# Kernel tuning notes

Hardware: AMD Instinct MI355X
Metric: run time of the kernel (lower is better)

Reference implementation:

```python
import jax, jax.numpy as jnp
import numpy as np

B, C, H, W = 8, 256, 64, 64
S = H * W  # dim_spatial = 4096
DQK = 256
DV = 256


def setup_inputs() -> dict:
    key = jax.random.key(0)
    k1, k2, k3, k4, k5 = jax.random.split(key, 5)
    queries = jax.random.normal(k1, (B, DQK, H, W), dtype=jnp.float32)
    keys = jax.random.normal(k2, (B, DQK, H, W), dtype=jnp.float32)
    values = jax.random.normal(k3, (B, DV, H, W), dtype=jnp.float32)
    q_pos = jax.random.normal(k4, (1, S, DQK), dtype=jnp.float32) * 0.05  # 'random_normal' init
    k_pos = jax.random.normal(k5, (1, S, DQK), dtype=jnp.float32) * 0.05
    return {"queries": queries, "keys": keys, "values": values, "q_pos": q_pos, "k_pos": k_pos}


def reference(queries, keys, values, q_pos, k_pos):
    scale = DQK ** (-0.5)
    # NCHW -> (B, S, C)
    q = jnp.transpose(queries, (0, 2, 3, 1)).reshape(-1, S, DQK) + q_pos
    k = jnp.transpose(keys, (0, 2, 3, 1)).reshape(-1, S, DQK) + k_pos
    v = jnp.transpose(values, (0, 2, 3, 1)).reshape(-1, S, DV)
    dots = jnp.einsum('bqd,bkd->bqk', q, k) * scale  # (B, S, S)
    attn = jax.nn.softmax(dots, axis=-1)
    out = jnp.einsum('bqk,bkd->bqd', attn, v)  # (B, S, DV)
    out = jnp.transpose(out, (0, 2, 1)).reshape(values.shape)  # (B, DV, H, W)
    return out
```

## Files before the change

### kernel.cpp

```cpp
#include <hip/hip_runtime.h>
#include <hip/hip_bf16.h>

#define B_N   8
#define S_N   4096
#define D_N   256
#define QBLK  64
#define KVBLK 64
#define SCALE 0.0625f

typedef __attribute__((ext_vector_type(8)))  short bf16x8;
typedef __attribute__((ext_vector_type(16))) float f32x16;

__device__ __forceinline__ void async16(const char* g, char* l) {
  __builtin_amdgcn_global_load_lds(
      (const __attribute__((address_space(1))) void*)g,
      (__attribute__((address_space(3))) void*)l, 16, 0, 0);
}

__device__ __forceinline__ unsigned cvt_pk_bf16(float lo, float hi) {
  unsigned r;
  asm("v_cvt_pk_bf16_f32 %0, %1, %2" : "=v"(r) : "v"(lo), "v"(hi));
  return r;
}
__device__ __forceinline__ void swap32(unsigned& a, unsigned& b) {
  asm("v_permlane32_swap_b32 %0, %1" : "+v"(a), "+v"(b));
}
__device__ __forceinline__ float xhalf_max(float x) {
  float a = x, b = x;
  asm("" : "+v"(b));
  asm("v_permlane32_swap_b32 %0, %1" : "+v"(a), "+v"(b));
  return fmaxf(a, b);
}
__device__ __forceinline__ float xhalf_add(float x) {
  float a = x, b = x;
  asm("" : "+v"(b));
  asm("v_permlane32_swap_b32 %0, %1" : "+v"(a), "+v"(b));
  return a + b;
}

__global__ void prep_qk(const float* __restrict__ src, const float* __restrict__ pos,
                        __hip_bfloat16* __restrict__ dst, float mul) {
  __shared__ float tile[64][65];
  const int b  = blockIdx.z;
  const int s0 = blockIdx.x * 64;
  const int c0 = blockIdx.y * 64;
  const int t  = threadIdx.x;
  const int x  = t & 63;
  const int y4 = t >> 6;
  const float* sp = src + ((size_t)b * D_N + c0) * S_N + s0;
#pragma unroll
  for (int i = 0; i < 16; ++i) {
    int c = y4 + i * 4;
    tile[c][x] = sp[(size_t)c * S_N + x];
  }
  __syncthreads();
  __hip_bfloat16* dp = dst + ((size_t)b * S_N + s0) * D_N + c0;
  const float* pp = pos + (size_t)s0 * D_N + c0;
#pragma unroll
  for (int i = 0; i < 16; ++i) {
    int s = y4 + i * 4;
    float v = (tile[x][s] + pp[(size_t)s * D_N + x]) * mul;
    dp[(size_t)s * D_N + x] = __float2bfloat16(v);
  }
}

struct alignas(8) bf4 { __hip_bfloat16 a, b, c, d; };
__global__ void prep_v(const float* __restrict__ src, __hip_bfloat16* __restrict__ dst) {
  size_t i = (size_t)blockIdx.x * blockDim.x + threadIdx.x;
  float4 v = reinterpret_cast<const float4*>(src)[i];
  bf4 o { __float2bfloat16(v.x), __float2bfloat16(v.y),
          __float2bfloat16(v.z), __float2bfloat16(v.w) };
  *reinterpret_cast<bf4*>(dst + i * 4) = o;
}

#define LDS_BYTES 65536

__global__ __launch_bounds__(128, 1) void attn_kernel(
    const __hip_bfloat16* __restrict__ Qb, const __hip_bfloat16* __restrict__ Kb,
    const __hip_bfloat16* __restrict__ Vtb, float* __restrict__ out) {
  __shared__ __align__(16) char lds[LDS_BYTES];

  const int tid  = threadIdx.x;
  const int wave = tid >> 6;
  const int lane = tid & 63;
  const int l31  = lane & 31;
  const int h    = lane >> 5;
  const int l7   = lane & 7;

  const int lin   = blockIdx.x;
  const int b     = lin & 7;
  const int qtile = lin >> 3;
  const int q0    = qtile * QBLK + wave * 32;

  bf16x8 qf[16];
  {
    const __hip_bfloat16* qp = Qb + ((size_t)b * S_N + q0 + l31) * D_N + h * 8;
#pragma unroll
    for (int kc = 0; kc < 16; ++kc)
      qf[kc] = *reinterpret_cast<const bf16x8*>(qp + kc * 16);
  }

  f32x16 o[8];
#pragma unroll
  for (int df = 0; df < 8; ++df)
#pragma unroll
    for (int r = 0; r < 16; ++r) o[df][r] = 0.f;
  float m_ = -1e30f, l_ = 0.f;

  char* Klds = lds;
  char* Vlds = lds + 32768;
  const char* kgbase = reinterpret_cast<const char*>(Kb  + (size_t)b * S_N * D_N);
  const char* vgbase = reinterpret_cast<const char*>(Vtb + (size_t)b * D_N * S_N);

  for (int t = 0; t < S_N / KVBLK; ++t) {
    __syncthreads();
    {
      const char* kt = kgbase + (size_t)t * KVBLK * (D_N * 2);
#pragma unroll
      for (int i = 0; i < 16; ++i) {
        int c    = wave * 16 + i;
        int T    = c * 1024 + lane * 16;
        int row  = T >> 9;
        int colb = T & 511;
        async16(kt + row * 512 + (colb ^ ((row & 7) << 4)), Klds + c * 1024);
      }
      const char* vt = vgbase + (size_t)t * KVBLK * 2;
#pragma unroll
      for (int i = 0; i < 16; ++i) {
        int c    = wave * 16 + i;
        int T    = c * 1024 + lane * 16;
        int d    = T >> 7;
        int colb = T & 127;
        async16(vt + (size_t)d * (S_N * 2) + (colb ^ ((d & 7) << 4)), Vlds + c * 1024);
      }
    }
    __syncthreads();

    f32x16 se[2];
#pragma unroll
    for (int e = 0; e < 2; ++e) {
#pragma unroll
      for (int r = 0; r < 16; ++r) se[e][r] = 0.f;
      const char* kr = Klds + (e * 32 + l31) * 512;
      const int swz = l7 << 4;
#pragma unroll
      for (int kc = 0; kc < 16; ++kc) {
        bf16x8 kf = *reinterpret_cast<const bf16x8*>(kr + ((kc * 32 + h * 16) ^ swz));
        se[e] = __builtin_amdgcn_mfma_f32_32x32x16_bf16(kf, qf[kc], se[e], 0, 0, 0);
      }
    }

    float t8[8];
#pragma unroll
    for (int i = 0; i < 8; ++i)
      t8[i] = fmaxf(fmaxf(se[0][i], se[0][i + 8]), fmaxf(se[1][i], se[1][i + 8]));
    float pm = fmaxf(fmaxf(fmaxf(t8[0], t8[1]), fmaxf(t8[2], t8[3])),
                     fmaxf(fmaxf(t8[4], t8[5]), fmaxf(t8[6], t8[7])));
    float pmax = xhalf_max(pm);

    if (!__all(pmax <= m_ + 8.f)) {
      float mn = fmaxf(m_, pmax);
      float al = __expf(m_ - mn);
      m_ = mn;
      l_ *= al;
#pragma unroll
      for (int df = 0; df < 8; ++df)
#pragma unroll
        for (int r = 0; r < 16; ++r) o[df][r] *= al;
    }
#pragma unroll
    for (int r = 0; r < 16; ++r) se[0][r] = __expf(se[0][r] - m_);
#pragma unroll
    for (int r = 0; r < 16; ++r) se[1][r] = __expf(se[1][r] - m_);
    float s8[8];
#pragma unroll
    for (int i = 0; i < 8; ++i)
      s8[i] = (se[0][i] + se[0][i + 8]) + (se[1][i] + se[1][i + 8]);
    float rs = ((s8[0] + s8[1]) + (s8[2] + s8[3])) + ((s8[4] + s8[5]) + (s8[6] + s8[7]));
    l_ += xhalf_add(rs);

    union U8 { unsigned u[4]; bf16x8 v; };
    U8 pb[4];
#pragma unroll
    for (int e = 0; e < 2; ++e) {
      unsigned u0 = cvt_pk_bf16(se[e][0],  se[e][1]);
      unsigned v0 = cvt_pk_bf16(se[e][4],  se[e][5]);
      swap32(u0, v0);
      unsigned u1 = cvt_pk_bf16(se[e][2],  se[e][3]);
      unsigned v1 = cvt_pk_bf16(se[e][6],  se[e][7]);
      swap32(u1, v1);
      pb[2 * e].u[0] = u0; pb[2 * e].u[1] = u1;
      pb[2 * e].u[2] = v0; pb[2 * e].u[3] = v1;
      unsigned u2 = cvt_pk_bf16(se[e][8],  se[e][9]);
      unsigned v2 = cvt_pk_bf16(se[e][12], se[e][13]);
      swap32(u2, v2);
      unsigned u3 = cvt_pk_bf16(se[e][10], se[e][11]);
      unsigned v3 = cvt_pk_bf16(se[e][14], se[e][15]);
      swap32(u3, v3);
      pb[2 * e + 1].u[0] = u2; pb[2 * e + 1].u[1] = u3;
      pb[2 * e + 1].u[2] = v2; pb[2 * e + 1].u[3] = v3;
    }

#pragma unroll
    for (int df = 0; df < 8; ++df) {
      const char* vr = Vlds + (df * 32 + l31) * 128;
      const int swz = l7 << 4;
#pragma unroll
      for (int kf = 0; kf < 4; ++kf) {
        bf16x8 vf = *reinterpret_cast<const bf16x8*>(vr + ((kf * 32 + h * 16) ^ swz));
        o[df] = __builtin_amdgcn_mfma_f32_32x32x16_bf16(vf, pb[kf].v, o[df], 0, 0, 0);
      }
    }
  }

  const float invl = 1.0f / l_;
  float* ob = out + (size_t)b * D_N * S_N + q0 + l31;
#pragma unroll
  for (int df = 0; df < 8; ++df)
#pragma unroll
    for (int r = 0; r < 16; ++r) {
      int d = df * 32 + (r & 3) + 8 * (r >> 2) + 4 * h;
      ob[(size_t)d * S_N] = o[df][r] * invl;
    }
}

extern "C" void kernel_launch(void* const* d_in, const int* in_sizes, int n_in,
                              void* d_out, int out_size, void* d_ws, size_t ws_size,
                              hipStream_t stream) {
  const float* queries = (const float*)d_in[0];
  const float* keys    = (const float*)d_in[1];
  const float* values  = (const float*)d_in[2];
  const float* q_pos   = (const float*)d_in[3];
  const float* k_pos   = (const float*)d_in[4];
  float* out = (float*)d_out;

  const size_t per = (size_t)B_N * S_N * D_N;
  __hip_bfloat16* Qb  = (__hip_bfloat16*)d_ws;
  __hip_bfloat16* Kb  = Qb + per;
  __hip_bfloat16* Vtb = Kb + per;

  prep_qk<<<dim3(S_N / 64, D_N / 64, B_N), 256, 0, stream>>>(queries, q_pos, Qb, SCALE);
  prep_qk<<<dim3(S_N / 64, D_N / 64, B_N), 256, 0, stream>>>(keys,    k_pos, Kb, 1.0f);
  prep_v <<<dim3((unsigned)(per / 4 / 256)), 256, 0, stream>>>(values, Vtb);
  attn_kernel<<<dim3((S_N / QBLK) * B_N), 128, 0, stream>>>(Qb, Kb, Vtb, out);
}
```

Measured before the change: 223.8 us.

## Split KV range across two wave teams per block and merge softmax partials

Each block now runs four waves in two teams: each team processes half of the key sequence with 32-key tiles, holding its own K/V buffers in LDS. At the end the teams exchange running max and sum through LDS, and team 0 rescales and combines both partial outputs before writing. The aim is more waves per CU and more latency hiding per query tile, at the cost of a cross-team reduction, smaller tiles that need more barriers per key, and higher register and LDS pressure. It also adds a new V swizzle layout and s_setprio around the MFMA sections.

Result: slower. 263.1 us (+17.6%).

```diff
diff --git a/kernel.cpp b/kernel.cpp
--- a/kernel.cpp
+++ b/kernel.cpp
@@ -5,7 +5,7 @@
 #define S_N   4096
 #define D_N   256
 #define QBLK  64
-#define KVBLK 64
+#define KVBLK 32
 #define SCALE 0.0625f
 
 typedef __attribute__((ext_vector_type(8)))  short bf16x8;
@@ -73,15 +73,17 @@
   *reinterpret_cast<bf4*>(dst + i * 4) = o;
 }
 
-#define LDS_BYTES 65536
-
-__global__ __launch_bounds__(128, 1) void attn_kernel(
+#define LDS_BYTES 66560
+
+__global__ __launch_bounds__(256, 2) void attn_kernel(
     const __hip_bfloat16* __restrict__ Qb, const __hip_bfloat16* __restrict__ Kb,
     const __hip_bfloat16* __restrict__ Vtb, float* __restrict__ out) {
   __shared__ __align__(16) char lds[LDS_BYTES];
 
   const int tid  = threadIdx.x;
   const int wave = tid >> 6;
+  const int team = wave >> 1;
+  const int w    = wave & 1;
   const int lane = tid & 63;
   const int l31  = lane & 31;
   const int h    = lane >> 5;
@@ -90,7 +92,8 @@
   const int lin   = blockIdx.x;
   const int b     = lin & 7;
   const int qtile = lin >> 3;
-  const int q0    = qtile * QBLK + wave * 32;
+  const int q0    = qtile * QBLK + w * 32;
+  const int K0    = team * (S_N / 2);
 
   bf16x8 qf[16];
   {
@@ -107,53 +110,56 @@
     for (int r = 0; r < 16; ++r) o[df][r] = 0.f;
   float m_ = -1e30f, l_ = 0.f;
 
-  char* Klds = lds;
-  char* Vlds = lds + 32768;
+  char* Klds = lds + team * 32768;
+  char* Vlds = Klds + 16384;
   const char* kgbase = reinterpret_cast<const char*>(Kb  + (size_t)b * S_N * D_N);
   const char* vgbase = reinterpret_cast<const char*>(Vtb + (size_t)b * D_N * S_N);
 
-  for (int t = 0; t < S_N / KVBLK; ++t) {
+  for (int t = 0; t < (S_N / 2) / KVBLK; ++t) {
+    const int key0 = K0 + t * KVBLK;
     __syncthreads();
     {
-      const char* kt = kgbase + (size_t)t * KVBLK * (D_N * 2);
-#pragma unroll
-      for (int i = 0; i < 16; ++i) {
-        int c    = wave * 16 + i;
+      const char* kt = kgbase + (size_t)key0 * (D_N * 2);
+#pragma unroll
+      for (int i = 0; i < 8; ++i) {
+        int c    = w * 8 + i;
         int T    = c * 1024 + lane * 16;
         int row  = T >> 9;
         int colb = T & 511;
         async16(kt + row * 512 + (colb ^ ((row & 7) << 4)), Klds + c * 1024);
       }
-      const char* vt = vgbase + (size_t)t * KVBLK * 2;
-#pragma unroll
-      for (int i = 0; i < 16; ++i) {
-        int c    = wave * 16 + i;
-        int T    = c * 1024 + lane * 16;
-        int d    = T >> 7;
-        int colb = T & 127;
-        async16(vt + (size_t)d * (S_N * 2) + (colb ^ ((d & 7) << 4)), Vlds + c * 1024);
+#pragma unroll
+      for (int i = 0; i < 8; ++i) {
+        int c  = w * 8 + i;
+        int T  = c * 1024 + lane * 16;
+        int r  = T >> 8;
+        int sp = (T >> 4) & 15;
+        int sl = sp ^ (r & 15);
+        int d  = r * 4 + (sl >> 2);
+        async16(vgbase + (size_t)d * (S_N * 2) + key0 * 2 + (sl & 3) * 16,
+                Vlds + c * 1024);
       }
     }
     __syncthreads();
 
-    f32x16 se[2];
-#pragma unroll
-    for (int e = 0; e < 2; ++e) {
-#pragma unroll
-      for (int r = 0; r < 16; ++r) se[e][r] = 0.f;
-      const char* kr = Klds + (e * 32 + l31) * 512;
+    f32x16 se;
+#pragma unroll
+    for (int r = 0; r < 16; ++r) se[r] = 0.f;
+    {
+      const char* kr = Klds + l31 * 512;
       const int swz = l7 << 4;
+      __builtin_amdgcn_s_setprio(1);
 #pragma unroll
       for (int kc = 0; kc < 16; ++kc) {
         bf16x8 kf = *reinterpret_cast<const bf16x8*>(kr + ((kc * 32 + h * 16) ^ swz));
-        se[e] = __builtin_amdgcn_mfma_f32_32x32x16_bf16(kf, qf[kc], se[e], 0, 0, 0);
-      }
+        se = __builtin_amdgcn_mfma_f32_32x32x16_bf16(kf, qf[kc], se, 0, 0, 0);
+      }
+      __builtin_amdgcn_s_setprio(0);
     }
 
     float t8[8];
 #pragma unroll
-    for (int i = 0; i < 8; ++i)
-      t8[i] = fmaxf(fmaxf(se[0][i], se[0][i + 8]), fmaxf(se[1][i], se[1][i + 8]));
+    for (int i = 0; i < 8; ++i) t8[i] = fmaxf(se[i], se[i + 8]);
     float pm = fmaxf(fmaxf(fmaxf(t8[0], t8[1]), fmaxf(t8[2], t8[3])),
                      fmaxf(fmaxf(t8[4], t8[5]), fmaxf(t8[6], t8[7])));
     float pmax = xhalf_max(pm);
@@ -169,59 +175,82 @@
         for (int r = 0; r < 16; ++r) o[df][r] *= al;
     }
 #pragma unroll
-    for (int r = 0; r < 16; ++r) se[0][r] = __expf(se[0][r] - m_);
-#pragma unroll
-    for (int r = 0; r < 16; ++r) se[1][r] = __expf(se[1][r] - m_);
+    for (int r = 0; r < 16; ++r) se[r] = __expf(se[r] - m_);
     float s8[8];
 #pragma unroll
-    for (int i = 0; i < 8; ++i)
-      s8[i] = (se[0][i] + se[0][i + 8]) + (se[1][i] + se[1][i + 8]);
+    for (int i = 0; i < 8; ++i) s8[i] = se[i] + se[i + 8];
     float rs = ((s8[0] + s8[1]) + (s8[2] + s8[3])) + ((s8[4] + s8[5]) + (s8[6] + s8[7]));
     l_ += xhalf_add(rs);
 
     union U8 { unsigned u[4]; bf16x8 v; };
-    U8 pb[4];
-#pragma unroll
-    for (int e = 0; e < 2; ++e) {
-      unsigned u0 = cvt_pk_bf16(se[e][0],  se[e][1]);
-      unsigned v0 = cvt_pk_bf16(se[e][4],  se[e][5]);
+    U8 pb[2];
+    {
+      unsigned u0 = cvt_pk_bf16(se[0],  se[1]);
+      unsigned v0 = cvt_pk_bf16(se[4],  se[5]);
       swap32(u0, v0);
-      unsigned u1 = cvt_pk_bf16(se[e][2],  se[e][3]);
-      unsigned v1 = cvt_pk_bf16(se[e][6],  se[e][7]);
+      unsigned u1 = cvt_pk_bf16(se[2],  se[3]);
+      unsigned v1 = cvt_pk_bf16(se[6],  se[7]);
       swap32(u1, v1);
-      pb[2 * e].u[0] = u0; pb[2 * e].u[1] = u1;
-      pb[2 * e].u[2] = v0; pb[2 * e].u[3] = v1;
-      unsigned u2 = cvt_pk_bf16(se[e][8],  se[e][9]);
-      unsigned v2 = cvt_pk_bf16(se[e][12], se[e][13]);
+      pb[0].u[0] = u0; pb[0].u[1] = u1; pb[0].u[2] = v0; pb[0].u[3] = v1;
+      unsigned u2 = cvt_pk_bf16(se[8],  se[9]);
+      unsigned v2 = cvt_pk_bf16(se[12], se[13]);
       swap32(u2, v2);
-      unsigned u3 = cvt_pk_bf16(se[e][10], se[e][11]);
-      unsigned v3 = cvt_pk_bf16(se[e][14], se[e][15]);
+      unsigned u3 = cvt_pk_bf16(se[10], se[11]);
+      unsigned v3 = cvt_pk_bf16(se[14], se[15]);
       swap32(u3, v3);
-      pb[2 * e + 1].u[0] = u2; pb[2 * e + 1].u[1] = u3;
-      pb[2 * e + 1].u[2] = v2; pb[2 * e + 1].u[3] = v3;
-    }
-
+      pb[1].u[0] = u2; pb[1].u[1] = u3; pb[1].u[2] = v2; pb[1].u[3] = v3;
+    }
+
+    __builtin_amdgcn_s_setprio(1);
 #pragma unroll
     for (int df = 0; df < 8; ++df) {
-      const char* vr = Vlds + (df * 32 + l31) * 128;
-      const int swz = l7 << 4;
-#pragma unroll
-      for (int kf = 0; kf < 4; ++kf) {
-        bf16x8 vf = *reinterpret_cast<const bf16x8*>(vr + ((kf * 32 + h * 16) ^ swz));
+      const int rr = df * 8 + (l31 >> 2);
+      const char* vr = Vlds + rr * 256;
+      const int rx = ((df & 1) * 8) + (l31 >> 2);
+#pragma unroll
+      for (int kf = 0; kf < 2; ++kf) {
+        int sl = (l31 & 3) * 4 + kf * 2 + h;
+        int sp = sl ^ rx;
+        bf16x8 vf = *reinterpret_cast<const bf16x8*>(vr + sp * 16);
         o[df] = __builtin_amdgcn_mfma_f32_32x32x16_bf16(vf, pb[kf].v, o[df], 0, 0, 0);
       }
     }
-  }
-
-  const float invl = 1.0f / l_;
-  float* ob = out + (size_t)b * D_N * S_N + q0 + l31;
-#pragma unroll
-  for (int df = 0; df < 8; ++df)
-#pragma unroll
-    for (int r = 0; r < 16; ++r) {
-      int d = df * 32 + (r & 3) + 8 * (r >> 2) + 4 * h;
-      ob[(size_t)d * S_N] = o[df][r] * invl;
-    }
+    __builtin_amdgcn_s_setprio(0);
+  }
+
+  float2* mlb = reinterpret_cast<float2*>(lds + 65536);
+  if (h == 0) mlb[wave * 32 + l31] = make_float2(m_, l_);
+  __syncthreads();
+  float2 pml = mlb[(wave ^ 2) * 32 + l31];
+  float mstar = fmaxf(m_, pml.x);
+  float c     = __expf(m_ - mstar);
+
+  if (team == 1) {
+    float* obuf = reinterpret_cast<float*>(lds + w * 32768);
+#pragma unroll
+    for (int df = 0; df < 8; ++df)
+#pragma unroll
+      for (int r = 0; r < 16; ++r) {
+        int d = df * 32 + (r & 3) + 8 * (r >> 2) + 4 * h;
+        obuf[d * 32 + l31] = o[df][r] * c;
+      }
+  }
+  __syncthreads();
+  if (team == 0) {
+    float cp    = __expf(pml.x - mstar);
+    float lstar = c * l_ + pml.y;
+    lstar = c * l_ + cp * pml.y;
+    float inv   = 1.0f / lstar;
+    const float* obuf = reinterpret_cast<const float*>(lds + w * 32768);
+    float* ob = out + (size_t)b * D_N * S_N + q0 + l31;
+#pragma unroll
+    for (int df = 0; df < 8; ++df)
+#pragma unroll
+      for (int r = 0; r < 16; ++r) {
+        int d = df * 32 + (r & 3) + 8 * (r >> 2) + 4 * h;
+        ob[(size_t)d * S_N] = (o[df][r] * c + obuf[d * 32 + l31]) * inv;
+      }
+  }
 }
 
 extern "C" void kernel_launch(void* const* d_in, const int* in_sizes, int n_in,
@@ -242,5 +271,5 @@
   prep_qk<<<dim3(S_N / 64, D_N / 64, B_N), 256, 0, stream>>>(queries, q_pos, Qb, SCALE);
   prep_qk<<<dim3(S_N / 64, D_N / 64, B_N), 256, 0, stream>>>(keys,    k_pos, Kb, 1.0f);
   prep_v <<<dim3((unsigned)(per / 4 / 256)), 256, 0, stream>>>(values, Vtb);
-  attn_kernel<<<dim3((S_N / QBLK) * B_N), 128, 0, stream>>>(Qb, Kb, Vtb, out);
-}
+  attn_kernel<<<dim3((S_N / QBLK) * B_N), 256, 0, stream>>>(Qb, Kb, Vtb, out);
+}
```

## Double-buffer K/V tiles in LDS and widen query block to four waves

Applied to the files above, without the earlier changes.

The attention kernel now processes 128 queries per block with 256 threads (four waves). It double-buffers the K/V tiles in 128 KB of LDS: the next tile's async global-to-LDS loads are issued before the current tile is computed, and completion is tracked with explicit vmcnt waits and barriers. K loading is split across two waves and V loading across the other two. This aims to hide global load latency behind MFMA work and to share each K/V tile among more query waves. In exchange it needs twice the LDS per block, so only one block fits per CU and the grid has half as many blocks.

Measured after the change: 418.4 us. 1.87x slower.

```diff
diff --git a/kernel.cpp b/kernel.cpp
--- a/kernel.cpp
+++ b/kernel.cpp
@@ -4,8 +4,9 @@
 #define B_N   8
 #define S_N   4096
 #define D_N   256
-#define QBLK  64
+#define QBLK  128
 #define KVBLK 64
+#define NT    (S_N / KVBLK)
 #define SCALE 0.0625f
 
 typedef __attribute__((ext_vector_type(8)))  short bf16x8;
@@ -73,9 +74,9 @@
   *reinterpret_cast<bf4*>(dst + i * 4) = o;
 }
 
-#define LDS_BYTES 65536
-
-__global__ __launch_bounds__(128, 1) void attn_kernel(
+#define LDS_BYTES 131072
+
+__global__ __launch_bounds__(256, 1) void attn_kernel(
     const __hip_bfloat16* __restrict__ Qb, const __hip_bfloat16* __restrict__ Kb,
     const __hip_bfloat16* __restrict__ Vtb, float* __restrict__ out) {
   __shared__ __align__(16) char lds[LDS_BYTES];
@@ -107,14 +108,12 @@
     for (int r = 0; r < 16; ++r) o[df][r] = 0.f;
   float m_ = -1e30f, l_ = 0.f;
 
-  char* Klds = lds;
-  char* Vlds = lds + 32768;
   const char* kgbase = reinterpret_cast<const char*>(Kb  + (size_t)b * S_N * D_N);
   const char* vgbase = reinterpret_cast<const char*>(Vtb + (size_t)b * D_N * S_N);
 
-  for (int t = 0; t < S_N / KVBLK; ++t) {
-    __syncthreads();
-    {
+  auto STAGE = [&](int buf, int t) {
+    char* base = lds + buf * 65536;
+    if (wave < 2) {
       const char* kt = kgbase + (size_t)t * KVBLK * (D_N * 2);
 #pragma unroll
       for (int i = 0; i < 16; ++i) {
@@ -122,19 +121,36 @@
         int T    = c * 1024 + lane * 16;
         int row  = T >> 9;
         int colb = T & 511;
-        async16(kt + row * 512 + (colb ^ ((row & 7) << 4)), Klds + c * 1024);
-      }
+        async16(kt + row * 512 + (colb ^ ((row & 7) << 4)), base + c * 1024);
+      }
+    } else {
       const char* vt = vgbase + (size_t)t * KVBLK * 2;
 #pragma unroll
       for (int i = 0; i < 16; ++i) {
-        int c    = wave * 16 + i;
+        int c    = (wave - 2) * 16 + i;
         int T    = c * 1024 + lane * 16;
         int d    = T >> 7;
         int colb = T & 127;
-        async16(vt + (size_t)d * (S_N * 2) + (colb ^ ((d & 7) << 4)), Vlds + c * 1024);
-      }
-    }
-    __syncthreads();
+        async16(vt + (size_t)d * (S_N * 2) + (colb ^ ((d & 7) << 4)),
+                base + 32768 + c * 1024);
+      }
+    }
+  };
+
+  STAGE(0, 0);
+
+  for (int t = 0; t < NT; ++t) {
+    const int cur = t & 1;
+    if (t + 1 < NT) {
+      STAGE(cur ^ 1, t + 1);
+      asm volatile("s_waitcnt vmcnt(16)" ::: "memory");
+    } else {
+      asm volatile("s_waitcnt vmcnt(0)" ::: "memory");
+    }
+    __builtin_amdgcn_s_barrier();
+
+    const char* Klds = lds + cur * 65536;
+    const char* Vlds = Klds + 32768;
 
     f32x16 se[2];
 #pragma unroll
@@ -211,6 +227,8 @@
         o[df] = __builtin_amdgcn_mfma_f32_32x32x16_bf16(vf, pb[kf].v, o[df], 0, 0, 0);
       }
     }
+
+    __builtin_amdgcn_s_barrier();
   }
 
   const float invl = 1.0f / l_;
@@ -242,5 +260,5 @@
   prep_qk<<<dim3(S_N / 64, D_N / 64, B_N), 256, 0, stream>>>(queries, q_pos, Qb, SCALE);
   prep_qk<<<dim3(S_N / 64, D_N / 64, B_N), 256, 0, stream>>>(keys,    k_pos, Kb, 1.0f);
   prep_v <<<dim3((unsigned)(per / 4 / 256)), 256, 0, stream>>>(values, Vtb);
-  attn_kernel<<<dim3((S_N / QBLK) * B_N), 128, 0, stream>>>(Qb, Kb, Vtb, out);
-}
+  attn_kernel<<<dim3((S_N / QBLK) * B_N), 256, 0, stream>>>(Qb, Kb, Vtb, out);
+}
```

## Drop LDS staging, load K/V fragments directly into registers with double buffering

Applied to the files above, without the earlier changes.

The attention kernel now runs one wave per block covering 32 queries and 32 keys per step. It loads K and V fragments straight from global memory into registers, and prefetches the next K chunk into a ping-pong register buffer. This removes the LDS staging and the __syncthreads barriers. The cost is that K/V are no longer shared between waves through LDS, so each wave reads K/V from global/L2 on its own, and register pressure rises. Output stores are switched to nontemporal.

Result: slower. 487.6 us (+117.9%).

```diff
diff --git a/kernel.cpp b/kernel.cpp
--- a/kernel.cpp
+++ b/kernel.cpp
@@ -4,18 +4,12 @@
 #define B_N   8
 #define S_N   4096
 #define D_N   256
-#define QBLK  64
-#define KVBLK 64
+#define QW    32
+#define NC    128
 #define SCALE 0.0625f
 
 typedef __attribute__((ext_vector_type(8)))  short bf16x8;
 typedef __attribute__((ext_vector_type(16))) float f32x16;
-
-__device__ __forceinline__ void async16(const char* g, char* l) {
-  __builtin_amdgcn_global_load_lds(
-      (const __attribute__((address_space(1))) void*)g,
-      (__attribute__((address_space(3))) void*)l, 16, 0, 0);
-}
 
 __device__ __forceinline__ unsigned cvt_pk_bf16(float lo, float hi) {
   unsigned r;
@@ -73,24 +67,97 @@
   *reinterpret_cast<bf4*>(dst + i * 4) = o;
 }
 
-#define LDS_BYTES 65536
-
-__global__ __launch_bounds__(128, 1) void attn_kernel(
+
+#define BODY(KCUR, KNXT, C) do {                                               \
+    const int c_ = (C);                                                        \
+                               \
+    bf16x8 vf[16];                                                             \
+    _Pragma("unroll")                                                          \
+    for (int df = 0; df < 8; ++df)                                             \
+      _Pragma("unroll")                                                        \
+      for (int k2 = 0; k2 < 2; ++k2)                                           \
+        vf[df * 2 + k2] = *reinterpret_cast<const bf16x8*>(                    \
+            vb + (size_t)(df * 32 + l31) * 8192 + c_ * 64 + k2 * 32 + h * 16); \
+                                            \
+    const int cn_ = (c_ + 1 < NC) ? c_ + 1 : 0;                                \
+    _Pragma("unroll")                                                          \
+    for (int kc = 0; kc < 16; ++kc)                                            \
+      KNXT[kc] = *reinterpret_cast<const bf16x8*>(                             \
+          kb + (size_t)(cn_ * 32 + l31) * 512 + kc * 32 + h * 16);             \
+                             \
+    f32x16 se;                                                                 \
+    _Pragma("unroll")                                                          \
+    for (int r = 0; r < 16; ++r) se[r] = 0.f;                                  \
+    _Pragma("unroll")                                                          \
+    for (int kc = 0; kc < 16; ++kc)                                            \
+      se = __builtin_amdgcn_mfma_f32_32x32x16_bf16(KCUR[kc], qf[kc], se, 0, 0, 0); \
+                      \
+    float t8[8];                                                               \
+    _Pragma("unroll")                                                          \
+    for (int i = 0; i < 8; ++i) t8[i] = fmaxf(se[i], se[i + 8]);               \
+    float pm = fmaxf(fmaxf(fmaxf(t8[0], t8[1]), fmaxf(t8[2], t8[3])),          \
+                     fmaxf(fmaxf(t8[4], t8[5]), fmaxf(t8[6], t8[7])));         \
+    float pmax = xhalf_max(pm);                                                \
+    if (!__all(pmax <= m_ + 8.f)) {                             \
+      float mn = fmaxf(m_, pmax);                                              \
+      float al = __expf(m_ - mn);                                              \
+      m_ = mn;                                                                 \
+      l_ *= al;                                                                \
+      _Pragma("unroll")                                                        \
+      for (int df = 0; df < 8; ++df)                                           \
+        _Pragma("unroll")                                                      \
+        for (int r = 0; r < 16; ++r) o[df][r] *= al;                           \
+    }                                                                          \
+    _Pragma("unroll")                                                          \
+    for (int r = 0; r < 16; ++r) se[r] = __expf(se[r] - m_);                   \
+    float s8[8];                                                               \
+    _Pragma("unroll")                                                          \
+    for (int i = 0; i < 8; ++i) s8[i] = se[i] + se[i + 8];                     \
+    float rs = ((s8[0] + s8[1]) + (s8[2] + s8[3])) +                           \
+               ((s8[4] + s8[5]) + (s8[6] + s8[7]));                            \
+    l_ += xhalf_add(rs);                                                       \
+                   \
+    union U8 { unsigned u[4]; bf16x8 v; };                                     \
+    U8 pb[2];                                                                  \
+    {                                                                          \
+      unsigned u0 = cvt_pk_bf16(se[0],  se[1]);                                \
+      unsigned v0 = cvt_pk_bf16(se[4],  se[5]);                                \
+      swap32(u0, v0);                                                          \
+      unsigned u1 = cvt_pk_bf16(se[2],  se[3]);                                \
+      unsigned v1 = cvt_pk_bf16(se[6],  se[7]);                                \
+      swap32(u1, v1);                                                          \
+      pb[0].u[0] = u0; pb[0].u[1] = u1; pb[0].u[2] = v0; pb[0].u[3] = v1;      \
+      unsigned u2 = cvt_pk_bf16(se[8],  se[9]);                                \
+      unsigned v2 = cvt_pk_bf16(se[12], se[13]);                               \
+      swap32(u2, v2);                                                          \
+      unsigned u3 = cvt_pk_bf16(se[10], se[11]);                               \
+      unsigned v3 = cvt_pk_bf16(se[14], se[15]);                               \
+      swap32(u3, v3);                                                          \
+      pb[1].u[0] = u2; pb[1].u[1] = u3; pb[1].u[2] = v2; pb[1].u[3] = v3;      \
+    }                                                                          \
+                              \
+    _Pragma("unroll")                                                          \
+    for (int df = 0; df < 8; ++df)                                             \
+      _Pragma("unroll")                                                        \
+      for (int k2 = 0; k2 < 2; ++k2)                                           \
+        o[df] = __builtin_amdgcn_mfma_f32_32x32x16_bf16(vf[df * 2 + k2],       \
+                                                        pb[k2].v, o[df], 0, 0, 0); \
+  } while (0)
+
+__global__ __launch_bounds__(64, 1) void attn_kernel(
     const __hip_bfloat16* __restrict__ Qb, const __hip_bfloat16* __restrict__ Kb,
     const __hip_bfloat16* __restrict__ Vtb, float* __restrict__ out) {
-  __shared__ __align__(16) char lds[LDS_BYTES];
-
-  const int tid  = threadIdx.x;
-  const int wave = tid >> 6;
-  const int lane = tid & 63;
+  const int lane = threadIdx.x & 63;
   const int l31  = lane & 31;
   const int h    = lane >> 5;
-  const int l7   = lane & 7;
-
-  const int lin   = blockIdx.x;
-  const int b     = lin & 7;
-  const int qtile = lin >> 3;
-  const int q0    = qtile * QBLK + wave * 32;
+
+  const int lin = blockIdx.x;
+  const int b   = lin & 7;
+  const int qt  = lin >> 3;
+  const int q0  = qt * QW;
+
+  const char* kb = reinterpret_cast<const char*>(Kb  + (size_t)b * S_N * D_N);
+  const char* vb = reinterpret_cast<const char*>(Vtb + (size_t)b * D_N * S_N);
 
   bf16x8 qf[16];
   {
@@ -107,120 +174,25 @@
     for (int r = 0; r < 16; ++r) o[df][r] = 0.f;
   float m_ = -1e30f, l_ = 0.f;
 
-  char* Klds = lds;
-  char* Vlds = lds + 32768;
-  const char* kgbase = reinterpret_cast<const char*>(Kb  + (size_t)b * S_N * D_N);
-  const char* vgbase = reinterpret_cast<const char*>(Vtb + (size_t)b * D_N * S_N);
-
-  for (int t = 0; t < S_N / KVBLK; ++t) {
-    __syncthreads();
-    {
-      const char* kt = kgbase + (size_t)t * KVBLK * (D_N * 2);
-#pragma unroll
-      for (int i = 0; i < 16; ++i) {
-        int c    = wave * 16 + i;
-        int T    = c * 1024 + lane * 16;
-        int row  = T >> 9;
-        int colb = T & 511;
-        async16(kt + row * 512 + (colb ^ ((row & 7) << 4)), Klds + c * 1024);
-      }
-      const char* vt = vgbase + (size_t)t * KVBLK * 2;
-#pragma unroll
-      for (int i = 0; i < 16; ++i) {
-        int c    = wave * 16 + i;
-        int T    = c * 1024 + lane * 16;
-        int d    = T >> 7;
-        int colb = T & 127;
-        async16(vt + (size_t)d * (S_N * 2) + (colb ^ ((d & 7) << 4)), Vlds + c * 1024);
-      }
-    }
-    __syncthreads();
-
-    f32x16 se[2];
-#pragma unroll
-    for (int e = 0; e < 2; ++e) {
-#pragma unroll
-      for (int r = 0; r < 16; ++r) se[e][r] = 0.f;
-      const char* kr = Klds + (e * 32 + l31) * 512;
-      const int swz = l7 << 4;
-#pragma unroll
-      for (int kc = 0; kc < 16; ++kc) {
-        bf16x8 kf = *reinterpret_cast<const bf16x8*>(kr + ((kc * 32 + h * 16) ^ swz));
-        se[e] = __builtin_amdgcn_mfma_f32_32x32x16_bf16(kf, qf[kc], se[e], 0, 0, 0);
-      }
-    }
-
-    float t8[8];
-#pragma unroll
-    for (int i = 0; i < 8; ++i)
-      t8[i] = fmaxf(fmaxf(se[0][i], se[0][i + 8]), fmaxf(se[1][i], se[1][i + 8]));
-    float pm = fmaxf(fmaxf(fmaxf(t8[0], t8[1]), fmaxf(t8[2], t8[3])),
-                     fmaxf(fmaxf(t8[4], t8[5]), fmaxf(t8[6], t8[7])));
-    float pmax = xhalf_max(pm);
-
-    if (!__all(pmax <= m_ + 8.f)) {
-      float mn = fmaxf(m_, pmax);
-      float al = __expf(m_ - mn);
-      m_ = mn;
-      l_ *= al;
-#pragma unroll
-      for (int df = 0; df < 8; ++df)
-#pragma unroll
-        for (int r = 0; r < 16; ++r) o[df][r] *= al;
-    }
-#pragma unroll
-    for (int r = 0; r < 16; ++r) se[0][r] = __expf(se[0][r] - m_);
-#pragma unroll
-    for (int r = 0; r < 16; ++r) se[1][r] = __expf(se[1][r] - m_);
-    float s8[8];
-#pragma unroll
-    for (int i = 0; i < 8; ++i)
-      s8[i] = (se[0][i] + se[0][i + 8]) + (se[1][i] + se[1][i + 8]);
-    float rs = ((s8[0] + s8[1]) + (s8[2] + s8[3])) + ((s8[4] + s8[5]) + (s8[6] + s8[7]));
-    l_ += xhalf_add(rs);
-
-    union U8 { unsigned u[4]; bf16x8 v; };
-    U8 pb[4];
-#pragma unroll
-    for (int e = 0; e < 2; ++e) {
-      unsigned u0 = cvt_pk_bf16(se[e][0],  se[e][1]);
-      unsigned v0 = cvt_pk_bf16(se[e][4],  se[e][5]);
-      swap32(u0, v0);
-      unsigned u1 = cvt_pk_bf16(se[e][2],  se[e][3]);
-      unsigned v1 = cvt_pk_bf16(se[e][6],  se[e][7]);
-      swap32(u1, v1);
-      pb[2 * e].u[0] = u0; pb[2 * e].u[1] = u1;
-      pb[2 * e].u[2] = v0; pb[2 * e].u[3] = v1;
-      unsigned u2 = cvt_pk_bf16(se[e][8],  se[e][9]);
-      unsigned v2 = cvt_pk_bf16(se[e][12], se[e][13]);
-      swap32(u2, v2);
-      unsigned u3 = cvt_pk_bf16(se[e][10], se[e][11]);
-      unsigned v3 = cvt_pk_bf16(se[e][14], se[e][15]);
-      swap32(u3, v3);
-      pb[2 * e + 1].u[0] = u2; pb[2 * e + 1].u[1] = u3;
-      pb[2 * e + 1].u[2] = v2; pb[2 * e + 1].u[3] = v3;
-    }
-
-#pragma unroll
-    for (int df = 0; df < 8; ++df) {
-      const char* vr = Vlds + (df * 32 + l31) * 128;
-      const int swz = l7 << 4;
-#pragma unroll
-      for (int kf = 0; kf < 4; ++kf) {
-        bf16x8 vf = *reinterpret_cast<const bf16x8*>(vr + ((kf * 32 + h * 16) ^ swz));
-        o[df] = __builtin_amdgcn_mfma_f32_32x32x16_bf16(vf, pb[kf].v, o[df], 0, 0, 0);
-      }
-    }
-  }
-
-  const float invl = 1.0f / l_;
+  bf16x8 kfA[16], kfB[16];
+#pragma unroll
+  for (int kc = 0; kc < 16; ++kc)
+    kfA[kc] = *reinterpret_cast<const bf16x8*>(
+        kb + (size_t)l31 * 512 + kc * 32 + h * 16);
+
+  for (int c = 0; c < NC; c += 2) {
+    BODY(kfA, kfB, c);
+    BODY(kfB, kfA, c + 1);
+  }
+
+  const float inv = 1.0f / l_;
   float* ob = out + (size_t)b * D_N * S_N + q0 + l31;
 #pragma unroll
   for (int df = 0; df < 8; ++df)
 #pragma unroll
     for (int r = 0; r < 16; ++r) {
       int d = df * 32 + (r & 3) + 8 * (r >> 2) + 4 * h;
-      ob[(size_t)d * S_N] = o[df][r] * invl;
+      __builtin_nontemporal_store(o[df][r] * inv, ob + (size_t)d * S_N);
     }
 }
 
@@ -242,5 +214,5 @@
   prep_qk<<<dim3(S_N / 64, D_N / 64, B_N), 256, 0, stream>>>(queries, q_pos, Qb, SCALE);
   prep_qk<<<dim3(S_N / 64, D_N / 64, B_N), 256, 0, stream>>>(keys,    k_pos, Kb, 1.0f);
   prep_v <<<dim3((unsigned)(per / 4 / 256)), 256, 0, stream>>>(values, Vtb);
-  attn_kernel<<<dim3((S_N / QBLK) * B_N), 128, 0, stream>>>(Qb, Kb, Vtb, out);
-}
+  attn_kernel<<<dim3((S_N / QW) * B_N), 64, 0, stream>>>(Qb, Kb, Vtb, out);
+}
```
